# Kernel optimization log

Hardware: AMD Instinct MI355X
Metric: run time of the kernel (lower is better)

Reference implementation:

```python
import jax, jax.numpy as jnp
import numpy as np

B, T, D = 1, 2048, 1024
H, HD, NH = 16, 64, 2        # heads, head_dim, num_householder
EPS = 1e-5                   # RMSNorm eps
SCALE = HD ** -0.5           # query scale (k_dim**-0.5)


def setup_inputs() -> dict:
    key = jax.random.key(0)
    ks = jax.random.split(key, 10)
    init = lambda k, shape: jax.random.normal(k, shape, jnp.float32) * (shape[0] ** -0.5)
    return {
        "x": jax.random.normal(ks[0], (B, T, D), jnp.float32),
        "Wq": init(ks[1], (D, H * HD)),
        "Wk": init(ks[2], (D, NH * H * HD)),
        "Wv": init(ks[3], (D, NH * H * HD)),
        "Wb": init(ks[4], (D, NH * H)),
        "Wa": init(ks[5], (D, H)),
        "A_log": jnp.log(jax.random.uniform(ks[6], (H,), jnp.float32, 1e-2, 16.0)),
        "dt_bias": jnp.zeros((H,), jnp.float32),
        "Wg": init(ks[7], (D, H * HD)),
        "norm_weight": jnp.ones((HD,), jnp.float32),
        "Wo": init(ks[8], (H * HD, D)),
    }


def _l2norm(t):
    return t * jax.lax.rsqrt(jnp.sum(t * t, -1, keepdims=True) + 1e-6)


def _forward(x, Wq, Wk, Wv, Wb, Wa, A_log, dt_bias, Wg, norm_weight, Wo):
    # projections; householder sub-steps interleaved along time -> length T*NH
    q = _l2norm((x @ Wq).reshape(B, T, H, HD)) * SCALE            # [B,T,H,HD]
    k = _l2norm((x @ Wk).reshape(B, T, NH, H, HD)).reshape(B, T * NH, H, HD)
    v = (x @ Wv).reshape(B, T * NH, H, HD)
    # allow_neg_eigval=True -> beta in (0,2)
    beta = 2.0 * jax.nn.sigmoid((x @ Wb).reshape(B, T * NH, H))
    # gated decay applied once per token (first sub-step), zeros for the rest
    g = -jnp.exp(A_log) * jax.nn.softplus(x @ Wa + dt_bias)       # [B,T,H]
    g = jnp.concatenate(
        [g[:, :, None], jnp.zeros((B, T, NH - 1, H), g.dtype)], axis=2
    ).reshape(B, T * NH, H)
    qf = jnp.repeat(q, NH, axis=1)  # only sub-step NH-1 outputs are kept

    def step(S, inp):
        # S: [B,H,HD_k,HD_v] recurrent state
        k_t, v_t, b_t, g_t, q_t = inp
        S = S * jnp.exp(g_t)[..., None, None]
        pred = jnp.einsum('bhk,bhkv->bhv', k_t, S)
        dv = (v_t - pred) * b_t[..., None]
        S = S + k_t[..., None] * dv[..., None, :]
        o = jnp.einsum('bhk,bhkv->bhv', q_t, S)
        return S, o

    tm = lambda a: jnp.swapaxes(a, 0, 1)  # time-major for scan
    S0 = jnp.zeros((B, H, HD, HD), x.dtype)
    _, o = jax.lax.scan(step, S0, (tm(k), tm(v), tm(beta), tm(g), tm(qf)))
    o = tm(o[NH - 1::NH])  # last householder sub-step per token -> [B,T,H,HD]

    # gated RMSNorm (FusedRMSNormGated with swish gate)
    o = o * jax.lax.rsqrt(jnp.mean(o * o, -1, keepdims=True) + EPS) * norm_weight
    gate = (x @ Wg).reshape(B, T, H, HD)
    o = o * (gate * jax.nn.sigmoid(gate))
    return o.reshape(B, T, H * HD) @ Wo


def reference(x, Wq, Wk, Wv, Wb, Wa, A_log, dt_bias, Wg, norm_weight, Wo):
    return _forward(x, Wq, Wk, Wv, Wb, Wa, A_log, dt_bias, Wg, norm_weight, Wo)
```

## Files before the change

kernel.cpp:

```cpp
#include <hip/hip_runtime.h>
#include <stdint.h>


typedef unsigned short u16;
typedef __attribute__((ext_vector_type(8))) short bf16x8;
typedef __attribute__((ext_vector_type(4))) float f32x4;
typedef __attribute__((ext_vector_type(2))) float f32x2;
typedef __attribute__((ext_vector_type(4))) unsigned short u16x4;

#define TT 2048
#define NP 6208
#define NC 64
#define CS 64

__device__ __forceinline__ u16 f2bf(float f) {
  union { float f; uint32_t u; } v; v.f = f;
  uint32_t r = v.u + 0x7fffu + ((v.u >> 16) & 1u);
  return (u16)(r >> 16);
}
__device__ __forceinline__ float bf2f(u16 b) {
  union { uint32_t u; float f; } v; v.u = ((uint32_t)b) << 16; return v.f;
}

__device__ __forceinline__ void gload_lds16(const u16* g, u16* l) {
  __builtin_amdgcn_global_load_lds(
      (__attribute__((address_space(1))) const void*)(uintptr_t)g,
      (__attribute__((address_space(3))) void*)(uint32_t)(uintptr_t)l, 16, 0, 0);
}

__global__ void cvt_kernel(const float* __restrict__ src, u16* __restrict__ dst, long n) {
  long i = (long)blockIdx.x * 256 + threadIdx.x;
  if (i < n) dst[i] = f2bf(src[i]);
}

__global__ __launch_bounds__(256) void transAll_kernel(
    const float* __restrict__ Wq, const float* __restrict__ Wk,
    const float* __restrict__ Wv, const float* __restrict__ Wb,
    const float* __restrict__ Wa, const float* __restrict__ Wg,
    const float* __restrict__ Wo, u16* __restrict__ WT, u16* __restrict__ WoT) {
  int bx = blockIdx.x;
  const float* src; u16* dst; int cols;
  if      (bx < 32)  { src = Wq; dst = WT;                cols = 1024; }
  else if (bx < 96)  { src = Wk; dst = WT + 1024UL*1024;  cols = 2048; bx -= 32; }
  else if (bx < 160) { src = Wv; dst = WT + 3072UL*1024;  cols = 2048; bx -= 96; }
  else if (bx < 161) { src = Wb; dst = WT + 5120UL*1024;  cols = 32;   bx -= 160; }
  else if (bx < 162) { src = Wa; dst = WT + 5152UL*1024;  cols = 16;   bx -= 161; }
  else if (bx < 194) { src = Wg; dst = WT + 5168UL*1024;  cols = 1024; bx -= 162; }
  else               { src = Wo; dst = WoT;               cols = 1024; bx -= 194; }
  __shared__ float tile[32][33];
  const int tx = threadIdx.x & 31, ty = threadIdx.x >> 5;
  const int c0 = bx * 32, r0 = blockIdx.y * 32;
  for (int rr = ty; rr < 32; rr += 8)
    if (c0 + tx < cols) tile[rr][tx] = src[(size_t)(r0 + rr) * cols + c0 + tx];
  __syncthreads();
  for (int rr = ty; rr < 32; rr += 8)
    if (c0 + rr < cols) dst[(size_t)(c0 + rr) * 1024 + r0 + tx] = f2bf(tile[tx][rr]);
}

__global__ __launch_bounds__(256) void beacon_kernel(float* __restrict__ out, int n) {
  int i = blockIdx.x * 256 + threadIdx.x;
  if (i < n) out[i] = 4000.0f;
}

__global__ __launch_bounds__(256) void gemm128(const u16* __restrict__ A,
    const u16* __restrict__ BT, float* __restrict__ Cf, u16* __restrict__ Cb,
    int K, int lda, int ldc, int Nmax, int out_bf16) {
  const int bm = blockIdx.x * 128, bn = blockIdx.y * 128;
  const int tid = threadIdx.x, w = tid >> 6, lane = tid & 63;
  const int wr = (w >> 1) * 64, wc = (w & 1) * 64;
  const int quad = lane >> 4, r = lane & 15;
  __shared__ u16 As[128][32], Bs[128][32];
  f32x4 acc[4][4] = {};
  const int sr = w * 32 + (lane >> 2);
  const int sc = (lane & 3) * 8;
  const u16* gA0 = A  + (size_t)(bm + sr) * lda + sc;
  const u16* gA1 = A  + (size_t)(bm + sr + 16) * lda + sc;
  const u16* gB0 = BT + (size_t)(bn + sr) * K + sc;
  const u16* gB1 = BT + (size_t)(bn + sr + 16) * K + sc;
  u16* lA0 = &As[w * 32][0];
  u16* lA1 = &As[w * 32 + 16][0];
  u16* lB0 = &Bs[w * 32][0];
  u16* lB1 = &Bs[w * 32 + 16][0];
  for (int ks = 0; ks < K; ks += 32) {
    __syncthreads();
    gload_lds16(gA0 + ks, lA0);
    gload_lds16(gA1 + ks, lA1);
    gload_lds16(gB0 + ks, lB0);
    gload_lds16(gB1 + ks, lB1);
    __syncthreads();
    bf16x8 af[4], bf[4];
#pragma unroll
    for (int i = 0; i < 4; i++) af[i] = *(const bf16x8*)&As[wr + i * 16 + r][quad * 8];
#pragma unroll
    for (int j = 0; j < 4; j++) bf[j] = *(const bf16x8*)&Bs[wc + j * 16 + r][quad * 8];
#pragma unroll
    for (int i = 0; i < 4; i++)
#pragma unroll
      for (int j = 0; j < 4; j++)
        acc[i][j] = __builtin_amdgcn_mfma_f32_16x16x32_bf16(af[i], bf[j], acc[i][j], 0, 0, 0);
  }
#pragma unroll
  for (int i = 0; i < 4; i++)
#pragma unroll
    for (int j = 0; j < 4; j++)
#pragma unroll
      for (int rg = 0; rg < 4; rg++) {
        int row = bm + wr + i * 16 + quad * 4 + rg;
        int col = bn + wc + j * 16 + r;
        if (col < Nmax) {
          float v = acc[i][j][rg];
          if (out_bf16) Cb[(size_t)row * ldc + col] = f2bf(v);
          else          Cf[(size_t)row * ldc + col] = v;
        }
      }
}

__global__ __launch_bounds__(256) void prep_kernel(float* __restrict__ P,
    const float* __restrict__ A_log, const float* __restrict__ dt_bias,
    float* __restrict__ betab, float* __restrict__ gbuf) {
  const int t = blockIdx.x >> 2, w = threadIdx.x >> 6, lane = threadIdx.x & 63;
  const int h = (blockIdx.x & 3) * 4 + w;
  float* Pt = P + (size_t)t * NP;
  float qv = Pt[h * 64 + lane];
  float ss = qv * qv;
#pragma unroll
  for (int off = 32; off; off >>= 1) ss += __shfl_xor(ss, off);
  Pt[h * 64 + lane] = qv * rsqrtf(ss + 1e-6f) * 0.125f;
#pragma unroll
  for (int nh = 0; nh < 2; nh++) {
    float kv = Pt[1024 + nh * 1024 + h * 64 + lane];
    float ks = kv * kv;
#pragma unroll
    for (int off = 32; off; off >>= 1) ks += __shfl_xor(ks, off);
    Pt[1024 + nh * 1024 + h * 64 + lane] = kv * rsqrtf(ks + 1e-6f);
  }
  if (lane < 2) {
    float bb = Pt[5120 + lane * 16 + h];
    betab[(size_t)(2 * t + lane) * 16 + h] = 2.f / (1.f + expf(-bb));
  }
  if (lane == 0) {
    float a = Pt[5152 + h] + dt_bias[h];
    float sp = (a > 20.f) ? a : log1pf(expf(a));
    gbuf[t * 16 + h] = -expf(A_log[h]) * sp;
  }
}

__global__ __launch_bounds__(256, 1) void phaseA_kernel(const float* __restrict__ P,
    const float* __restrict__ betab, const float* __restrict__ gbuf,
    u16* __restrict__ Wbuf, u16* __restrict__ Uvbuf,
    float* __restrict__ Mbuf, float* __restrict__ NTbuf, float* __restrict__ cumbuf) {
  const int c = blockIdx.x, h = blockIdx.y, tid = threadIdx.x;
  const int bi = tid >> 4, bj = tid & 15;
  __shared__ float LA[64][68];
  __shared__ float LB[64][68];
  __shared__ float LC[64][68];
  __shared__ float cumch[64], betach[64], bbch[64], rowfl[64];
  const size_t base = ((size_t)c * 16 + h) * 4096;

  for (int e = tid; e < 4096; e += 256) {
    int i = e >> 6, d = e & 63, s = c * 64 + i, t = s >> 1, nh = s & 1;
    float kv = P[(size_t)t * NP + 1024 + nh * 1024 + h * 64 + d];
    LB[i][d] = kv; LA[d][i] = kv;
  }
  if (tid < 64) betach[tid] = betab[(size_t)(c * 64 + tid) * 16 + h];
  __syncthreads();
  if (tid == 0) {
    float cum = 0.f;
    for (int i = 0; i < 64; i++) {
      if ((i & 1) == 0) cum += gbuf[(c * 32 + (i >> 1)) * 16 + h];
      cumch[i] = cum;
    }
  }
  __syncthreads();
  if (tid < 64) {
    bbch[tid] = betach[tid] * expf(cumch[tid]);
    rowfl[tid] = expf(cumch[63] - cumch[tid]);
  }
  {
    float acc[4][4] = {};
#pragma unroll 4
    for (int d = 0; d < 64; d++) {
      f32x4 a = *(const f32x4*)&LA[d][4 * bi];
      f32x4 b = *(const f32x4*)&LA[d][4 * bj];
#pragma unroll
      for (int rr = 0; rr < 4; rr++)
#pragma unroll
        for (int cc = 0; cc < 4; cc++) acc[rr][cc] += a[rr] * b[cc];
    }
#pragma unroll
    for (int rr = 0; rr < 4; rr++)
#pragma unroll
      for (int cc = 0; cc < 4; cc++) {
        int i = 4 * bi + rr, j = 4 * bj + cc;
        LC[i][j] = (j < i) ? betach[i] * expf(cumch[i] - cumch[j]) * acc[rr][cc] : 0.f;
      }
  }
  __syncthreads();
  {
    int col = tid >> 2, part = tid & 3;
    if (part == 0) LA[col][0] = (col == 0) ? 1.f : 0.f;
    for (int i = 1; i < 64; i++) {
      float partial = 0.f;
      for (int j = col + part; j < i; j += 4) partial += LC[i][j] * LA[col][j];
      partial += __shfl_xor(partial, 1);
      partial += __shfl_xor(partial, 2);
      if (part == 0) LA[col][i] = ((i == col) ? 1.f : 0.f) - partial;
    }
  }
  __syncthreads();
  float vreg[16];
  {
    const int vi = tid >> 6, vd = tid & 63;
#pragma unroll
    for (int s = 0; s < 16; s++) {
      int i = vi + 4 * s, ss = c * 64 + i, t = ss >> 1, nh = ss & 1;
      vreg[s] = P[(size_t)t * NP + 3072 + nh * 1024 + h * 64 + vd];
    }
  }
  {
    float acc[4][4] = {};
#pragma unroll 4
    for (int j = 0; j < 4 * bi + 4; j++) {
      f32x4 tv = *(const f32x4*)&LA[j][4 * bi];
      f32x4 kv = *(const f32x4*)&LB[j][4 * bj];
      float bbj = bbch[j];
#pragma unroll
      for (int rr = 0; rr < 4; rr++)
#pragma unroll
        for (int cc = 0; cc < 4; cc++) acc[rr][cc] += tv[rr] * bbj * kv[cc];
    }
#pragma unroll
    for (int rr = 0; rr < 4; rr++) {
      int i = 4 * bi + rr;
      u16x4 wb;
#pragma unroll
      for (int cc = 0; cc < 4; cc++) { LC[i][4 * bj + cc] = acc[rr][cc]; wb[cc] = f2bf(acc[rr][cc]); }
      *(u16x4*)&Wbuf[base + (size_t)i * 64 + 4 * bj] = wb;
    }
  }
  __syncthreads();
  {
    const float bL = expf(cumch[63]);
    float acc[4][4] = {};
#pragma unroll 4
    for (int i = 0; i < 64; i++) {
      f32x4 kv = *(const f32x4*)&LB[i][4 * bi];
      f32x4 wv = *(const f32x4*)&LC[i][4 * bj];
      float rf = rowfl[i];
#pragma unroll
      for (int rr = 0; rr < 4; rr++)
#pragma unroll
        for (int cc = 0; cc < 4; cc++) acc[rr][cc] += rf * kv[rr] * wv[cc];
    }
#pragma unroll
    for (int rr = 0; rr < 4; rr++) {
      int m = 4 * bi + rr;
      f32x4 mv;
#pragma unroll
      for (int cc = 0; cc < 4; cc++)
        mv[cc] = ((m == 4 * bj + cc) ? bL : 0.f) - acc[rr][cc];
      *(f32x4*)&Mbuf[base + (size_t)m * 64 + 4 * bj] = mv;
    }
  }
  __syncthreads();
  {
    const int vi = tid >> 6, vd = tid & 63;
#pragma unroll
    for (int s = 0; s < 16; s++) LC[vi + 4 * s][vd] = vreg[s];
  }
  __syncthreads();
  float ua[4][4] = {};
  {
#pragma unroll 4
    for (int j = 0; j < 4 * bi + 4; j++) {
      f32x4 tv = *(const f32x4*)&LA[j][4 * bi];
      f32x4 vv = *(const f32x4*)&LC[j][4 * bj];
      float be = betach[j];
#pragma unroll
      for (int rr = 0; rr < 4; rr++)
#pragma unroll
        for (int cc = 0; cc < 4; cc++) ua[rr][cc] += tv[rr] * be * vv[cc];
    }
  }
  __syncthreads();
  {
#pragma unroll
    for (int rr = 0; rr < 4; rr++) {
      int i = 4 * bi + rr;
      u16x4 ub;
#pragma unroll
      for (int cc = 0; cc < 4; cc++) { LA[i][4 * bj + cc] = ua[rr][cc]; ub[cc] = f2bf(ua[rr][cc]); }
      *(u16x4*)&Uvbuf[base + (size_t)i * 64 + 4 * bj] = ub;
    }
  }
  __syncthreads();
  {
    float acc[4][4] = {};
#pragma unroll 4
    for (int i = 0; i < 64; i++) {
      f32x4 kv = *(const f32x4*)&LB[i][4 * bi];
      f32x4 uv = *(const f32x4*)&LA[i][4 * bj];
      float rf = rowfl[i];
#pragma unroll
      for (int rr = 0; rr < 4; rr++)
#pragma unroll
        for (int cc = 0; cc < 4; cc++) acc[rr][cc] += rf * kv[rr] * uv[cc];
    }
#pragma unroll
    for (int cc = 0; cc < 4; cc++) {
      f32x4 nv;
#pragma unroll
      for (int rr = 0; rr < 4; rr++) nv[rr] = acc[rr][cc];
      *(f32x4*)&NTbuf[base + (size_t)(4 * bj + cc) * 64 + 4 * bi] = nv;
    }
  }
  if (tid < 64) cumbuf[((size_t)c * 16 + h) * 64 + tid] = cumch[tid];
}

__global__ __launch_bounds__(128) void phaseB_kernel(const float* __restrict__ Mbuf,
    const float* __restrict__ NTbuf, u16* __restrict__ S0Tbuf) {
  const int g = blockIdx.x, h = blockIdx.y;
  const int tid = threadIdx.x, wv = tid >> 6, l = tid & 63;
  const int c0 = 4 * g + 2 * wv, c1 = c0 + 1;
  __shared__ float Ms[2][64][68];
  __shared__ float Ssh[2][4][64];
  float s0 = 0.f, s1 = 0.f;
  float n0, n1;
  f32x4 mn[8];
  {
    const float* Mc = Mbuf + (size_t)h * 4096;
#pragma unroll
    for (int i = 0; i < 8; i++) {
      int sl = tid * 8 + i;
      mn[i] = *(const f32x4*)(Mc + (sl >> 4) * 64 + (sl & 15) * 4);
    }
#pragma unroll
    for (int i = 0; i < 8; i++) {
      int sl = tid * 8 + i;
      *(f32x4*)&Ms[0][sl >> 4][(sl & 15) * 4] = mn[i];
    }
    const float* Nc = NTbuf + (size_t)h * 4096;
    n0 = Nc[c0 * 64 + l]; n1 = Nc[c1 * 64 + l];
  }
  Ssh[0][2 * wv][l] = 0.f; Ssh[0][2 * wv + 1][l] = 0.f;
  __syncthreads();
  int p = 0;
  for (int c = 0; c < NC; c++) {
    const size_t base = ((size_t)c * 16 + h) * 4096;
    S0Tbuf[base + (size_t)c0 * 64 + l] = f2bf(s0);
    S0Tbuf[base + (size_t)c1 * 64 + l] = f2bf(s1);
    float nn0 = 0.f, nn1 = 0.f;
    if (c + 1 < NC) {
      const float* Mn = Mbuf + ((size_t)(c + 1) * 16 + h) * 4096;
#pragma unroll
      for (int i = 0; i < 8; i++) {
        int sl = tid * 8 + i;
        mn[i] = *(const f32x4*)(Mn + (sl >> 4) * 64 + (sl & 15) * 4);
      }
      const float* Nn = NTbuf + ((size_t)(c + 1) * 16 + h) * 4096;
      nn0 = Nn[c0 * 64 + l]; nn1 = Nn[c1 * 64 + l];
    }
    float acc0 = n0, acc1 = n1;
#pragma unroll
    for (int q = 0; q < 16; q++) {
      f32x4 mv = *(const f32x4*)&Ms[p][l][4 * q];
      f32x4 sv0 = *(const f32x4*)&Ssh[p][2 * wv][4 * q];
      f32x4 sv1 = *(const f32x4*)&Ssh[p][2 * wv + 1][4 * q];
#pragma unroll
      for (int t = 0; t < 4; t++) { acc0 += mv[t] * sv0[t]; acc1 += mv[t] * sv1[t]; }
    }
    s0 = acc0; s1 = acc1;
    Ssh[p ^ 1][2 * wv][l] = s0; Ssh[p ^ 1][2 * wv + 1][l] = s1;
    if (c + 1 < NC) {
#pragma unroll
      for (int i = 0; i < 8; i++) {
        int sl = tid * 8 + i;
        *(f32x4*)&Ms[p ^ 1][sl >> 4][(sl & 15) * 4] = mn[i];
      }
    }
    __syncthreads();
    p ^= 1;
    n0 = nn0; n1 = nn1;
  }
}

__global__ __launch_bounds__(256) void phaseC_kernel(const float* __restrict__ P,
    const float* __restrict__ cumbuf, const u16* __restrict__ Wbuf,
    const u16* __restrict__ Uvbuf, const u16* __restrict__ S0Tbuf,
    const float* __restrict__ nw, u16* __restrict__ ybuf) {
  const int c = blockIdx.x, h = blockIdx.y, tid = threadIdx.x;
  const int rb = tid >> 4, jb = tid & 15;
  __shared__ float qT[64][36];
  __shared__ float kTc[64][68];
  __shared__ float Ul[64][68];
  __shared__ float PmT[64][36];
  __shared__ float cuml[64], nwl[64];
  const size_t base = (size_t)c * 16 + h;
  for (int e = tid; e < 2048; e += 256) {
    int r = e >> 6, d = e & 63;
    qT[d][r] = P[(size_t)(c * 32 + r) * NP + h * 64 + d];
  }
  for (int e = tid; e < 4096; e += 256) {
    int j = e >> 6, d = e & 63, s = c * 64 + j, t = s >> 1, nh = s & 1;
    kTc[d][j] = P[(size_t)t * NP + 1024 + nh * 1024 + h * 64 + d];
  }
  if (tid < 64) { cuml[tid] = cumbuf[base * 64 + tid]; nwl[tid] = nw[tid]; }
  __syncthreads();
  {
    float pa[2][4] = {};
#pragma unroll 4
    for (int d = 0; d < 64; d++) {
      f32x2 qv = *(const f32x2*)&qT[d][2 * rb];
      f32x4 kv = *(const f32x4*)&kTc[d][4 * jb];
#pragma unroll
      for (int rr = 0; rr < 2; rr++)
#pragma unroll
        for (int cc = 0; cc < 4; cc++) pa[rr][cc] += qv[rr] * kv[cc];
    }
#pragma unroll
    for (int rr = 0; rr < 2; rr++)
#pragma unroll
      for (int cc = 0; cc < 4; cc++) {
        int r = 2 * rb + rr, i = 2 * r + 1, j = 4 * jb + cc;
        PmT[j][r] = (j <= i) ? expf(cuml[i] - cuml[j]) * pa[rr][cc] : 0.f;
      }
  }
  __syncthreads();
  for (int e = tid; e < 4096; e += 256) {
    int i = e >> 6, m = e & 63;
    kTc[m][i] = bf2f(S0Tbuf[base * 4096 + e]);
    Ul[m][i]  = bf2f(Wbuf[base * 4096 + e]);
  }
  __syncthreads();
  float b2acc[4][4] = {};
  {
#pragma unroll 4
    for (int m = 0; m < 64; m++) {
      f32x4 wv = *(const f32x4*)&Ul[m][4 * rb];
      f32x4 sv = *(const f32x4*)&kTc[m][4 * jb];
#pragma unroll
      for (int rr = 0; rr < 4; rr++)
#pragma unroll
        for (int cc = 0; cc < 4; cc++) b2acc[rr][cc] += wv[rr] * sv[cc];
    }
  }
  __syncthreads();
#pragma unroll
  for (int rr = 0; rr < 4; rr++) {
    int i = 4 * rb + rr;
    u16x4 uv = *(const u16x4*)&Uvbuf[base * 4096 + (size_t)i * 64 + 4 * jb];
#pragma unroll
    for (int cc = 0; cc < 4; cc++)
      Ul[i][4 * jb + cc] = bf2f(f2bf(bf2f(uv[cc]) - b2acc[rr][cc]));
  }
  __syncthreads();
  float o[2][4];
  {
    float a1[2][4] = {}, a2[2][4] = {};
#pragma unroll 4
    for (int m = 0; m < 64; m++) {
      f32x2 qv = *(const f32x2*)&qT[m][2 * rb];
      f32x4 sv = *(const f32x4*)&kTc[m][4 * jb];
#pragma unroll
      for (int rr = 0; rr < 2; rr++)
#pragma unroll
        for (int cc = 0; cc < 4; cc++) a1[rr][cc] += qv[rr] * sv[cc];
    }
#pragma unroll 4
    for (int j = 0; j < 4 * rb + 4; j++) {
      f32x2 pv = *(const f32x2*)&PmT[j][2 * rb];
      f32x4 uv = *(const f32x4*)&Ul[j][4 * jb];
#pragma unroll
      for (int rr = 0; rr < 2; rr++)
#pragma unroll
        for (int cc = 0; cc < 4; cc++) a2[rr][cc] += pv[rr] * uv[cc];
    }
#pragma unroll
    for (int rr = 0; rr < 2; rr++) {
      float ec = expf(cuml[2 * (2 * rb + rr) + 1]);
#pragma unroll
      for (int cc = 0; cc < 4; cc++) o[rr][cc] = a1[rr][cc] * ec + a2[rr][cc];
    }
  }
  __syncthreads();
  float* ol = &qT[0][0];
#pragma unroll
  for (int rr = 0; rr < 2; rr++)
#pragma unroll
    for (int cc = 0; cc < 4; cc++)
      ol[(2 * rb + rr) * 68 + 4 * jb + cc] = o[rr][cc];
  __syncthreads();
  for (int e = tid; e < 2048; e += 256) {
    int r = e >> 6, d = e & 63;
    float ov = ol[r * 68 + d];
    float ss = ov * ov;
#pragma unroll
    for (int off = 32; off; off >>= 1) ss += __shfl_xor(ss, off);
    float on = ov * rsqrtf(ss * (1.f / 64.f) + 1e-5f) * nwl[d];
    int t = c * 32 + r;
    float gt = P[(size_t)t * NP + 5168 + h * 64 + d];
    float sw = gt / (1.f + expf(-gt));
    ybuf[(size_t)t * 1024 + h * 64 + d] = f2bf(on * sw);
  }
}

extern "C" void kernel_launch(void* const* d_in, const int* in_sizes, int n_in,
                              void* d_out, int out_size, void* d_ws, size_t ws_size,
                              hipStream_t stream) {
  const float* x       = (const float*)d_in[0];
  const float* Wq      = (const float*)d_in[1];
  const float* Wk      = (const float*)d_in[2];
  const float* Wv      = (const float*)d_in[3];
  const float* Wb      = (const float*)d_in[4];
  const float* Wa      = (const float*)d_in[5];
  const float* A_log   = (const float*)d_in[6];
  const float* dt_bias = (const float*)d_in[7];
  const float* Wg      = (const float*)d_in[8];
  const float* nw      = (const float*)d_in[9];
  const float* Wo      = (const float*)d_in[10];
  float* out = (float*)d_out;

  char* w = (char*)d_ws;
  size_t used = 0;
  auto alloc = [&](size_t bytes) {
    char* p = w + used; used += (bytes + 255) & ~(size_t)255; return p;
  };
  u16*   xb    = (u16*)  alloc(2048UL * 1024 * 2);
  u16*   WT    = (u16*)  alloc(6272UL * 1024 * 2);
  u16*   WoT   = (u16*)  alloc(1024UL * 1024 * 2);
  float* P     = (float*)alloc(2048UL * NP * 4);
  float* betab = (float*)alloc(4096UL * 16 * 4);
  float* gbuf  = (float*)alloc(2048UL * 16 * 4);
  u16*   ybuf  = (u16*)  alloc(2048UL * 1024 * 2);
  u16*   Wbuf  = (u16*)  alloc((size_t)NC * 16 * 4096 * 2);
  u16*   Uvbuf = (u16*)  alloc((size_t)NC * 16 * 4096 * 2);
  u16*   S0Tb  = (u16*)  alloc((size_t)NC * 16 * 4096 * 2);
  float* Mbuf  = (float*)alloc((size_t)NC * 16 * 4096 * 4);
  float* NTbuf = (float*)alloc((size_t)NC * 16 * 4096 * 4);
  float* cumb  = (float*)alloc((size_t)NC * 16 * 64 * 4);

  auto tgrid = [](long n) { return dim3((unsigned)((n + 255) / 256)); };
  if (used > ws_size) {
    beacon_kernel<<<tgrid(out_size), 256, 0, stream>>>(out, out_size);
    return;
  }

  hipMemsetAsync(WT + 6192UL * 1024, 0, 80UL * 1024 * 2, stream);

  cvt_kernel<<<tgrid(2048L*1024), 256, 0, stream>>>(x, xb, 2048L * 1024);
  transAll_kernel<<<dim3(226, 32), 256, 0, stream>>>(Wq, Wk, Wv, Wb, Wa, Wg, Wo, WT, WoT);

  gemm128<<<dim3(16, 49), 256, 0, stream>>>(xb, WT, P, nullptr, 1024, 1024, NP, NP, 0);
  prep_kernel<<<dim3(2048 * 4), 256, 0, stream>>>(P, A_log, dt_bias, betab, gbuf);

  phaseA_kernel<<<dim3(NC, 16), 256, 0, stream>>>(P, betab, gbuf, Wbuf, Uvbuf, Mbuf, NTbuf, cumb);
  phaseB_kernel<<<dim3(16, 16), 128, 0, stream>>>(Mbuf, NTbuf, S0Tb);
  phaseC_kernel<<<dim3(NC, 16), 256, 0, stream>>>(P, cumb, Wbuf, Uvbuf, S0Tb, nw, ybuf);

  gemm128<<<dim3(16, 8), 256, 0, stream>>>(ybuf, WoT, out, nullptr, 1024, 1024, 1024, 1024, 0);
}
```

Measured before the change: 400.7 us.

## Fuse q/k L2 norm into projection GEMM epilogue; use 64-row GEMM for output

Moves the per-head L2 normalization of q and k into the projection GEMM's epilogue, reducing across the 64 columns of each head with lane shuffles. This removes the separate pass that reread and rewrote the q/k sections of P. The leftover prep kernel now only computes beta and g. The output projection switches to a new 64x128-tile, 128-thread GEMM, which launches 256 blocks instead of 128 to fill more CUs.

```diff
diff --git a/kernel.cpp b/kernel.cpp
--- a/kernel.cpp
+++ b/kernel.cpp
@@ -64,7 +64,7 @@
 
 __global__ __launch_bounds__(256) void gemm128(const u16* __restrict__ A,
     const u16* __restrict__ BT, float* __restrict__ Cf, u16* __restrict__ Cb,
-    int K, int lda, int ldc, int Nmax, int out_bf16) {
+    int K, int lda, int ldc, int Nmax, int out_bf16, int do_norm) {
   const int bm = blockIdx.x * 128, bn = blockIdx.y * 128;
   const int tid = threadIdx.x, w = tid >> 6, lane = tid & 63;
   const int wr = (w >> 1) * 64, wc = (w & 1) * 64;
@@ -99,6 +99,29 @@
       for (int j = 0; j < 4; j++)
         acc[i][j] = __builtin_amdgcn_mfma_f32_16x16x32_bf16(af[i], bf[j], acc[i][j], 0, 0, 0);
   }
+  int mode = 0;
+  if (do_norm) { if (blockIdx.y < 8) mode = 1; else if (blockIdx.y < 24) mode = 2; }
+  if (mode) {
+#pragma unroll
+    for (int i = 0; i < 4; i++)
+#pragma unroll
+      for (int rg = 0; rg < 4; rg++) {
+        float a0 = acc[i][0][rg], a1 = acc[i][1][rg];
+        float a2 = acc[i][2][rg], a3 = acc[i][3][rg];
+        float ss = (a0 * a0 + a2 * a2) + (a1 * a1 + a3 * a3);
+        ss += __shfl_xor(ss, 8);
+        ss += __shfl_xor(ss, 4);
+        ss += __shfl_xor(ss, 2);
+        ss += __shfl_xor(ss, 1);
+        float rs = rsqrtf(ss + 1e-6f);
+#pragma unroll
+        for (int j = 0; j < 4; j++) {
+          float ov = acc[i][j][rg] * rs;
+          if (mode == 1) ov *= 0.125f;
+          acc[i][j][rg] = ov;
+        }
+      }
+  }
 #pragma unroll
   for (int i = 0; i < 4; i++)
 #pragma unroll
@@ -115,34 +138,66 @@
       }
 }
 
-__global__ __launch_bounds__(256) void prep_kernel(float* __restrict__ P,
+__global__ __launch_bounds__(128) void gemm64(const u16* __restrict__ A,
+    const u16* __restrict__ BT, float* __restrict__ C, int K, int lda, int ldc) {
+  const int bm = blockIdx.x * 64, bn = blockIdx.y * 128;
+  const int tid = threadIdx.x, w = tid >> 6, lane = tid & 63;
+  const int wc = w * 64;
+  const int quad = lane >> 4, r = lane & 15;
+  __shared__ u16 As[64][32], Bs[128][32];
+  f32x4 acc[4][4] = {};
+  const int lr = lane >> 2;
+  const int sc = (lane & 3) * 8;
+  for (int ks = 0; ks < K; ks += 32) {
+    __syncthreads();
+    if (w == 0) {
+      gload_lds16(A  + (size_t)(bm +  0 + lr) * lda + ks + sc, &As[0][0]);
+      gload_lds16(A  + (size_t)(bm + 16 + lr) * lda + ks + sc, &As[16][0]);
+      gload_lds16(A  + (size_t)(bm + 32 + lr) * lda + ks + sc, &As[32][0]);
+      gload_lds16(A  + (size_t)(bm + 48 + lr) * lda + ks + sc, &As[48][0]);
+      gload_lds16(BT + (size_t)(bn +  0 + lr) * K + ks + sc, &Bs[0][0]);
+      gload_lds16(BT + (size_t)(bn + 16 + lr) * K + ks + sc, &Bs[16][0]);
+    } else {
+      gload_lds16(BT + (size_t)(bn +  32 + lr) * K + ks + sc, &Bs[32][0]);
+      gload_lds16(BT + (size_t)(bn +  48 + lr) * K + ks + sc, &Bs[48][0]);
+      gload_lds16(BT + (size_t)(bn +  64 + lr) * K + ks + sc, &Bs[64][0]);
+      gload_lds16(BT + (size_t)(bn +  80 + lr) * K + ks + sc, &Bs[80][0]);
+      gload_lds16(BT + (size_t)(bn +  96 + lr) * K + ks + sc, &Bs[96][0]);
+      gload_lds16(BT + (size_t)(bn + 112 + lr) * K + ks + sc, &Bs[112][0]);
+    }
+    __syncthreads();
+    bf16x8 af[4], bf[4];
+#pragma unroll
+    for (int i = 0; i < 4; i++) af[i] = *(const bf16x8*)&As[i * 16 + r][quad * 8];
+#pragma unroll
+    for (int j = 0; j < 4; j++) bf[j] = *(const bf16x8*)&Bs[wc + j * 16 + r][quad * 8];
+#pragma unroll
+    for (int i = 0; i < 4; i++)
+#pragma unroll
+      for (int j = 0; j < 4; j++)
+        acc[i][j] = __builtin_amdgcn_mfma_f32_16x16x32_bf16(af[i], bf[j], acc[i][j], 0, 0, 0);
+  }
+#pragma unroll
+  for (int i = 0; i < 4; i++)
+#pragma unroll
+    for (int j = 0; j < 4; j++)
+#pragma unroll
+      for (int rg = 0; rg < 4; rg++)
+        C[(size_t)(bm + i * 16 + quad * 4 + rg) * ldc + bn + wc + j * 16 + r] = acc[i][j][rg];
+}
+
+__global__ __launch_bounds__(256) void prep_bg_kernel(const float* __restrict__ P,
     const float* __restrict__ A_log, const float* __restrict__ dt_bias,
     float* __restrict__ betab, float* __restrict__ gbuf) {
-  const int t = blockIdx.x >> 2, w = threadIdx.x >> 6, lane = threadIdx.x & 63;
-  const int h = (blockIdx.x & 3) * 4 + w;
-  float* Pt = P + (size_t)t * NP;
-  float qv = Pt[h * 64 + lane];
-  float ss = qv * qv;
-#pragma unroll
-  for (int off = 32; off; off >>= 1) ss += __shfl_xor(ss, off);
-  Pt[h * 64 + lane] = qv * rsqrtf(ss + 1e-6f) * 0.125f;
-#pragma unroll
-  for (int nh = 0; nh < 2; nh++) {
-    float kv = Pt[1024 + nh * 1024 + h * 64 + lane];
-    float ks = kv * kv;
-#pragma unroll
-    for (int off = 32; off; off >>= 1) ks += __shfl_xor(ks, off);
-    Pt[1024 + nh * 1024 + h * 64 + lane] = kv * rsqrtf(ks + 1e-6f);
-  }
-  if (lane < 2) {
-    float bb = Pt[5120 + lane * 16 + h];
-    betab[(size_t)(2 * t + lane) * 16 + h] = 2.f / (1.f + expf(-bb));
-  }
-  if (lane == 0) {
-    float a = Pt[5152 + h] + dt_bias[h];
-    float sp = (a > 20.f) ? a : log1pf(expf(a));
-    gbuf[t * 16 + h] = -expf(A_log[h]) * sp;
-  }
+  const int idx = blockIdx.x * 256 + threadIdx.x;
+  const int t = idx >> 4, h = idx & 15;
+  const float* Pt = P + (size_t)t * NP;
+  float b0 = Pt[5120 + h], b1 = Pt[5136 + h];
+  betab[(size_t)(2 * t) * 16 + h]     = 2.f / (1.f + expf(-b0));
+  betab[(size_t)(2 * t + 1) * 16 + h] = 2.f / (1.f + expf(-b1));
+  float a = Pt[5152 + h] + dt_bias[h];
+  float sp = (a > 20.f) ? a : log1pf(expf(a));
+  gbuf[t * 16 + h] = -expf(A_log[h]) * sp;
 }
 
 __global__ __launch_bounds__(256, 1) void phaseA_kernel(const float* __restrict__ P,
@@ -550,12 +605,12 @@
   cvt_kernel<<<tgrid(2048L*1024), 256, 0, stream>>>(x, xb, 2048L * 1024);
   transAll_kernel<<<dim3(226, 32), 256, 0, stream>>>(Wq, Wk, Wv, Wb, Wa, Wg, Wo, WT, WoT);
 
-  gemm128<<<dim3(16, 49), 256, 0, stream>>>(xb, WT, P, nullptr, 1024, 1024, NP, NP, 0);
-  prep_kernel<<<dim3(2048 * 4), 256, 0, stream>>>(P, A_log, dt_bias, betab, gbuf);
+  gemm128<<<dim3(16, 49), 256, 0, stream>>>(xb, WT, P, nullptr, 1024, 1024, NP, NP, 0, 1);
+  prep_bg_kernel<<<dim3(128), 256, 0, stream>>>(P, A_log, dt_bias, betab, gbuf);
 
   phaseA_kernel<<<dim3(NC, 16), 256, 0, stream>>>(P, betab, gbuf, Wbuf, Uvbuf, Mbuf, NTbuf, cumb);
   phaseB_kernel<<<dim3(16, 16), 128, 0, stream>>>(Mbuf, NTbuf, S0Tb);
   phaseC_kernel<<<dim3(NC, 16), 256, 0, stream>>>(P, cumb, Wbuf, Uvbuf, S0Tb, nw, ybuf);
 
-  gemm128<<<dim3(16, 8), 256, 0, stream>>>(ybuf, WoT, out, nullptr, 1024, 1024, 1024, 1024, 0);
-}
+  gemm64<<<dim3(32, 8), 128, 0, stream>>>(ybuf, WoT, out, 1024, 1024, 1024);
+}
```

Result: faster. 383.5 us (-4.3%).
